# Optimization experiments

Hardware: AMD Instinct MI355X
Metric: run time of the kernel (lower is better)

## Reference

```python
import jax, jax.numpy as jnp
import numpy as np

DILATED_KS = (7, 7)   # dilated_kernel_size (Hk, Wk)
SCALING = 1.0
GROUPS = 1
STRIDE = (1, 1)
PADDING = (3, 3)


def construct_kernel(weight, P):
    """Bilinear scatter-add of kernel_count weighted points into a dense
    (out, in//g, Hk, Wk) kernel. weight: (O, Cg, K), P: (2, Cg, K)."""
    Hk, Wk = DILATED_KS
    lim_h, lim_w = Hk // 2, Wk // 2
    O, Cg, K = weight.shape
    ph = jnp.clip(P[0] * SCALING, -lim_h, lim_h) + lim_h    # (Cg, K) in [0, Hk-1]
    pw = jnp.clip(P[1] * SCALING, -lim_w, lim_w) + lim_w    # (Cg, K) in [0, Wk-1]
    ih = jnp.floor(ph).astype(jnp.int32)
    iw = jnp.floor(pw).astype(jnp.int32)
    rh = ph - ih
    rw = pw - iw
    cidx = jnp.broadcast_to(jnp.arange(Cg)[:, None], (Cg, K))
    kern = jnp.zeros((O, Cg, Hk, Wk), dtype=weight.dtype)
    corners = [(0, 0, (1 - rh) * (1 - rw)),
               (0, 1, (1 - rh) * rw),
               (1, 0, rh * (1 - rw)),
               (1, 1, rh * rw)]
    for di, dj, frac in corners:
        # out-of-range corners (at the boundary) have zero frac; 'drop' discards them
        kern = kern.at[:, cidx, ih + di, iw + dj].add(weight * frac[None], mode='drop')
    return kern


def setup_inputs() -> dict:
    key = jax.random.key(0)
    k1, k2, k3, k4 = jax.random.split(key, 4)
    x = jax.random.normal(k1, (32, 128, 56, 56), dtype=jnp.float32)
    weight = jax.random.normal(k2, (128, 128, 9), dtype=jnp.float32) * 0.05
    P = jax.random.normal(k3, (2, 128, 9), dtype=jnp.float32)  # positions ~ N(0,1), clamped in fwd
    bias = jax.random.normal(k4, (128,), dtype=jnp.float32) * 0.05
    return {"x": x, "weight": weight, "P": P, "bias": bias}


def reference(x, weight, P, bias):
    kern = construct_kernel(weight, P)  # (O, Cg, 7, 7)
    out = jax.lax.conv_general_dilated(
        x, kern,
        window_strides=STRIDE,
        padding=[(PADDING[0], PADDING[0]), (PADDING[1], PADDING[1])],
        dimension_numbers=('NCHW', 'OIHW', 'NCHW'),
        feature_group_count=GROUPS)
    return out + bias[None, :, None, None]
```

## Files before the change

### kernel.cpp

```cpp
#include <hip/hip_runtime.h>
#include <stdint.h>

typedef short v8s __attribute__((ext_vector_type(8)));
typedef float v4f __attribute__((ext_vector_type(4)));

#define KS    7
#define KPTS  9
#define OCH   128
#define CCH   128
#define NB    32
#define HW    56
#define PAD   3

#define HBLK  4
#define ROWS  10
#define WP    72
#define CCK   32
#define NCC   4
#define HP    62
#define ROWB  (WP*CCK*2)
#define XS_B  (ROWS*WP*CCK*2)
#define AB_B  (4*OCH*CCK*2)
#define SMEM_B (XS_B + AB_B)
#define KB_BYTES ((size_t)NCC*49*OCH*CCK*2)

__device__ __forceinline__ unsigned short f2bf(float f) {
  unsigned int u = __builtin_bit_cast(unsigned int, f);
  u += 0x7fffu + ((u >> 16) & 1u);
  return (unsigned short)(u >> 16);
}

__device__ __forceinline__ void gl_lds16(const void* g, void* l) {
  __builtin_amdgcn_global_load_lds(
      (const __attribute__((address_space(1))) unsigned int*)g,
      (__attribute__((address_space(3))) unsigned int*)l, 16, 0, 0);
}

__global__ __launch_bounds__(128) void build_kern(
    const float* __restrict__ wgt, const float* __restrict__ P,
    unsigned short* __restrict__ kb) {
  __shared__ float sm[OCH*49];
  const int c = blockIdx.x, o = threadIdx.x;
  float* mine = &sm[o*49];
  #pragma unroll
  for (int j = 0; j < 49; ++j) mine[j] = 0.f;
  for (int k = 0; k < KPTS; ++k) {
    const float ph = fminf(fmaxf(P[c*KPTS + k], -3.f), 3.f) + 3.f;
    const float pw = fminf(fmaxf(P[CCH*KPTS + c*KPTS + k], -3.f), 3.f) + 3.f;
    const int ih = (int)floorf(ph), iw = (int)floorf(pw);
    const float rh = ph - (float)ih, rw = pw - (float)iw;
    const float wt = wgt[(o*CCH + c)*KPTS + k];
    mine[ih*KS + iw] += wt*(1.f-rh)*(1.f-rw);
    if (iw+1 < KS) mine[ih*KS + iw+1] += wt*(1.f-rh)*rw;
    if (ih+1 < KS) mine[(ih+1)*KS + iw] += wt*rh*(1.f-rw);
    if (ih+1 < KS && iw+1 < KS) mine[(ih+1)*KS + iw+1] += wt*rh*rw;
  }
  const int cc = c >> 5, sc = (c >> 3) & 3, cl = c & 7;
  const int pc = sc ^ ((o >> 1) & 3);
  for (int tap = 0; tap < 49; ++tap)
    kb[(((size_t)(cc*49 + tap)*OCH + o)*CCK) + pc*8 + cl] = f2bf(mine[tap]);
}

__global__ __launch_bounds__(256) void xpose(const float* __restrict__ x,
                                             unsigned short* __restrict__ xt) {
  __shared__ unsigned short lb[CCK][HW + 2];
  const int hp = blockIdx.x;
  const int cc = blockIdx.y;
  const int n  = blockIdx.z;
  const int t  = threadIdx.x;
  const int h  = hp - PAD;
  const bool valid = (unsigned)h < (unsigned)HW;
  if (valid) {
    const float* xb = x + ((size_t)(n*CCH + cc*CCK)*HW + h)*HW;
    #pragma unroll
    for (int k = 0; k < 7; ++k) {
      const int j = k*256 + t;
      const int c = j / HW, w = j % HW;
      lb[c][w] = f2bf(xb[(size_t)c*HW*HW + w]);
    }
  }
  __syncthreads();
  unsigned short* orow = xt + (size_t)((n*NCC + cc)*HP + hp)*(WP*CCK);
  for (int q = t; q < WP*4; q += 256) {
    const int wq = q >> 2, pc = q & 3;
    const int s  = pc ^ ((wq >> 1) & 3);
    v8s v = (v8s){0,0,0,0,0,0,0,0};
    const int w = wq - PAD;
    if (valid && (unsigned)w < (unsigned)HW) {
      #pragma unroll
      for (int jj = 0; jj < 8; ++jj) v[jj] = (short)lb[s*8 + jj][w];
    }
    *(v8s*)&orow[wq*CCK + pc*8] = v;
  }
}

#define MFMA_TAP(FA, FB)                                                      \
  __builtin_amdgcn_s_setprio(1);                                              \
  _Pragma("unroll")                                                           \
  for (int nt = 0; nt < 4; ++nt) {                                            \
    _Pragma("unroll")                                                         \
    for (int mt = 0; mt < 8; ++mt)                                            \
      acc[mt][nt] = __builtin_amdgcn_mfma_f32_16x16x32_bf16(FA[mt], FB[nt],   \
                                                            acc[mt][nt], 0, 0, 0); \
  }                                                                           \
  __builtin_amdgcn_s_setprio(0);

__global__ __launch_bounds__(256, 2) void dcls_conv(
    const unsigned short* __restrict__ xt, const unsigned short* __restrict__ kb,
    const float* __restrict__ bias, float* __restrict__ out)
{
  extern __shared__ char smem[];
  unsigned short* xs = (unsigned short*)smem;
  unsigned short* ab = (unsigned short*)(smem + XS_B);

  const int n   = blockIdx.x;
  const int hb  = blockIdx.y;
  const int tid = threadIdx.x;
  const int lane = tid & 63;
  const int wv   = tid >> 6;
  const int col  = lane & 15;
  const int kgrp = lane >> 4;
  const int swA  = (kgrp ^ ((col >> 1) & 3)) << 3;

  v4f acc[8][4];
  #pragma unroll
  for (int m = 0; m < 8; ++m)
    #pragma unroll
    for (int t = 0; t < 4; ++t)
      acc[m][t] = (v4f){0.f,0.f,0.f,0.f};

  v8s fa0[8], fa1[8], fb0[4], fb1[4];

  for (int cc = 0; cc < NCC; ++cc) {
    const char* src = (const char*)xt + (size_t)((n*NCC + cc)*HP + hb*HBLK)*ROWB;
    for (int i = wv; i < 45; i += 4)
      gl_lds16(src + i*1024 + lane*16, (char*)xs + i*1024);
    const char* ks = (const char*)kb + (size_t)cc*49*8192;
    #pragma unroll
    for (int u = 0; u < 2; ++u)
      #pragma unroll
      for (int j = 0; j < 2; ++j)
        gl_lds16(ks + u*8192 + wv*2048 + j*1024 + lane*16,
                 (char*)ab + u*8192 + wv*2048 + j*1024);
    __syncthreads();

    #pragma unroll
    for (int mt = 0; mt < 8; ++mt)
      fa0[mt] = *(const v8s*)&ab[(mt*16 + col)*CCK + swA];
    {
      const int swB = (kgrp ^ ((col >> 1) & 3)) << 3;
      const int base = (wv*WP + col)*CCK + swB;
      #pragma unroll
      for (int nt = 0; nt < 4; ++nt)
        fb0[nt] = *(const v8s*)&xs[base + nt*512];
    }

    for (int phx = 0; phx < 24; ++phx) {
      const int t0 = 2*phx;
      {
        const int tp = t0 + 2;
        #pragma unroll
        for (int j = 0; j < 2; ++j)
          gl_lds16(ks + (size_t)tp*8192 + wv*2048 + j*1024 + lane*16,
                   (char*)ab + (size_t)(tp & 3)*8192 + wv*2048 + j*1024);
        const int tq = t0 + 3;
        if (tq < 49) {
          #pragma unroll
          for (int j = 0; j < 2; ++j)
            gl_lds16(ks + (size_t)tq*8192 + wv*2048 + j*1024 + lane*16,
                     (char*)ab + (size_t)(tq & 3)*8192 + wv*2048 + j*1024);
        }
      }
      {
        const int t = t0 + 1, kh = t/7, kw = t - kh*7, r = wv + kh;
        const unsigned short* ap = ab + (size_t)(t & 3)*(OCH*CCK);
        #pragma unroll
        for (int mt = 0; mt < 8; ++mt)
          fa1[mt] = *(const v8s*)&ap[(mt*16 + col)*CCK + swA];
        const int swB = (kgrp ^ (((col + kw) >> 1) & 3)) << 3;
        const int base = (r*WP + col + kw)*CCK + swB;
        #pragma unroll
        for (int nt = 0; nt < 4; ++nt)
          fb1[nt] = *(const v8s*)&xs[base + nt*512];
      }
      MFMA_TAP(fa0, fb0)
      {
        const int t = t0 + 2, kh = t/7, kw = t - kh*7, r = wv + kh;
        const int swB = (kgrp ^ (((col + kw) >> 1) & 3)) << 3;
        const int base = (r*WP + col + kw)*CCK + swB;
        #pragma unroll
        for (int nt = 0; nt < 4; ++nt)
          fb0[nt] = *(const v8s*)&xs[base + nt*512];
      }
      MFMA_TAP(fa1, fb1)
      __syncthreads();
      {
        const unsigned short* ap = ab + (size_t)((t0 + 2) & 3)*(OCH*CCK);
        #pragma unroll
        for (int mt = 0; mt < 8; ++mt)
          fa0[mt] = *(const v8s*)&ap[(mt*16 + col)*CCK + swA];
      }
    }
    MFMA_TAP(fa0, fb0)
    __syncthreads();
  }

  const int h = hb*HBLK + wv;
  #pragma unroll
  for (int mt = 0; mt < 8; ++mt) {
    #pragma unroll
    for (int rr = 0; rr < 4; ++rr) {
      const int o = mt*16 + (lane >> 4)*4 + rr;
      const float bs = bias[o];
      #pragma unroll
      for (int nt = 0; nt < 4; ++nt) {
        const int w = nt*16 + col;
        if (w < HW)
          out[((size_t)(n*OCH + o)*HW + h)*HW + w] = acc[mt][nt][rr] + bs;
      }
    }
  }
}

extern "C" void kernel_launch(void* const* d_in, const int* in_sizes, int n_in,
                              void* d_out, int out_size, void* d_ws, size_t ws_size,
                              hipStream_t stream) {
  const float* x    = (const float*)d_in[0];
  const float* wgt  = (const float*)d_in[1];
  const float* P    = (const float*)d_in[2];
  const float* bias = (const float*)d_in[3];
  float* out = (float*)d_out;

  unsigned short* kb = (unsigned short*)d_ws;
  unsigned short* xt = (unsigned short*)((char*)d_ws + (2u<<20));

  hipFuncSetAttribute((const void*)dcls_conv,
                      hipFuncAttributeMaxDynamicSharedMemorySize, SMEM_B);

  build_kern<<<CCH, OCH, 0, stream>>>(wgt, P, kb);
  xpose<<<dim3(HP, NCC, NB), 256, 0, stream>>>(x, xt);
  dcls_conv<<<dim3(NB, HW/HBLK), 256, SMEM_B, stream>>>(xt, kb, bias, out);
}
```

Measured before the change: 159.3 us.

## Switch conv to 32x32x16 MFMA with 8-wave blocks and register-streamed weights

Replaces the 16x16x32 bf16 MFMA tiling with 32x32x16 MFMA, doubles the rows per block to 8 with 512 threads, and prefetches the per-tap weight fragments straight from global memory into registers in an MFMA-ready layout instead of staging them through LDS with per-tap barriers. The weight builder emits that fragment-ordered layout. The goal is to cut LDS traffic and synchronisation in the inner tap loop and raise MFMA efficiency. The cost is exposed global-load latency on weight fragments, more registers, and only 224 blocks in the grid.

```diff
diff --git a/kernel.cpp b/kernel.cpp
--- a/kernel.cpp
+++ b/kernel.cpp
@@ -1,8 +1,8 @@
 #include <hip/hip_runtime.h>
 #include <stdint.h>
 
-typedef short v8s __attribute__((ext_vector_type(8)));
-typedef float v4f __attribute__((ext_vector_type(4)));
+typedef short v8s  __attribute__((ext_vector_type(8)));
+typedef float v16f __attribute__((ext_vector_type(16)));
 
 #define KS    7
 #define KPTS  9
@@ -12,17 +12,14 @@
 #define HW    56
 #define PAD   3
 
-#define HBLK  4
-#define ROWS  10
+#define HBLK  8
+#define ROWS  14
 #define WP    72
 #define CCK   32
 #define NCC   4
 #define HP    62
 #define ROWB  (WP*CCK*2)
-#define XS_B  (ROWS*WP*CCK*2)
-#define AB_B  (4*OCH*CCK*2)
-#define SMEM_B (XS_B + AB_B)
-#define KB_BYTES ((size_t)NCC*49*OCH*CCK*2)
+#define SMEM_B 65536
 
 __device__ __forceinline__ unsigned short f2bf(float f) {
   unsigned int u = __builtin_bit_cast(unsigned int, f);
@@ -55,10 +52,12 @@
     if (ih+1 < KS) mine[(ih+1)*KS + iw] += wt*rh*(1.f-rw);
     if (ih+1 < KS && iw+1 < KS) mine[(ih+1)*KS + iw+1] += wt*rh*rw;
   }
-  const int cc = c >> 5, sc = (c >> 3) & 3, cl = c & 7;
-  const int pc = sc ^ ((o >> 1) & 3);
+  const int cc = c >> 5, c32 = c & 31;
+  const int ks = c32 >> 4, g = (c32 >> 3) & 1, j = c & 7;
+  const int mt = o >> 5, l5 = o & 31;
+  const size_t base = ((size_t)cc*49*8 + ks*4 + mt)*512 + (g*32 + l5)*8 + j;
   for (int tap = 0; tap < 49; ++tap)
-    kb[(((size_t)(cc*49 + tap)*OCH + o)*CCK) + pc*8 + cl] = f2bf(mine[tap]);
+    kb[base + (size_t)tap*4096] = f2bf(mine[tap]);
 }
 
 __global__ __launch_bounds__(256) void xpose(const float* __restrict__ x,
@@ -94,129 +93,102 @@
   }
 }
 
-#define MFMA_TAP(FA, FB)                                                      \
-  __builtin_amdgcn_s_setprio(1);                                              \
-  _Pragma("unroll")                                                           \
-  for (int nt = 0; nt < 4; ++nt) {                                            \
+#define TAP_BODY(T, CUR, NXT, PF)                                             \
+  {                                                                           \
+    const int kh = (T)/7, kw = (T) - kh*7;                                    \
+    if (PF) {                                                                 \
+      const unsigned short* kn = kt + (size_t)((T)+1)*4096;                   \
+      _Pragma("unroll")                                                       \
+      for (int f = 0; f < 8; ++f)                                             \
+        NXT[f] = *(const v8s*)&kn[f*512 + lane*8];                            \
+    }                                                                         \
+    const int r = wv + kh;                                                    \
+    v8s bf[2][2];                                                             \
     _Pragma("unroll")                                                         \
-    for (int mt = 0; mt < 8; ++mt)                                            \
-      acc[mt][nt] = __builtin_amdgcn_mfma_f32_16x16x32_bf16(FA[mt], FB[nt],   \
-                                                            acc[mt][nt], 0, 0, 0); \
-  }                                                                           \
-  __builtin_amdgcn_s_setprio(0);
-
-__global__ __launch_bounds__(256, 2) void dcls_conv(
+    for (int nt = 0; nt < 2; ++nt) {                                          \
+      const int w = nt*32 + l5 + kw;                                          \
+      const int xw = (w >> 1) & 3;                                            \
+      _Pragma("unroll")                                                       \
+      for (int ks = 0; ks < 2; ++ks) {                                        \
+        const int phys = (ks*2 + g) ^ xw;                                     \
+        bf[nt][ks] = *(const v8s*)&xs[(r*WP + w)*CCK + phys*8];               \
+      }                                                                       \
+    }                                                                         \
+    __builtin_amdgcn_s_setprio(1);                                            \
+    _Pragma("unroll")                                                         \
+    for (int ks = 0; ks < 2; ++ks)                                            \
+      _Pragma("unroll")                                                       \
+      for (int mt = 0; mt < 4; ++mt)                                          \
+        _Pragma("unroll")                                                     \
+        for (int nt = 0; nt < 2; ++nt)                                        \
+          acc[mt][nt] = __builtin_amdgcn_mfma_f32_32x32x16_bf16(              \
+              CUR[ks*4 + mt], bf[nt][ks], acc[mt][nt], 0, 0, 0);              \
+    __builtin_amdgcn_s_setprio(0);                                            \
+  }
+
+__global__ __launch_bounds__(512, 2) void dcls_conv(
     const unsigned short* __restrict__ xt, const unsigned short* __restrict__ kb,
     const float* __restrict__ bias, float* __restrict__ out)
 {
   extern __shared__ char smem[];
   unsigned short* xs = (unsigned short*)smem;
-  unsigned short* ab = (unsigned short*)(smem + XS_B);
 
   const int n   = blockIdx.x;
   const int hb  = blockIdx.y;
   const int tid = threadIdx.x;
   const int lane = tid & 63;
   const int wv   = tid >> 6;
-  const int col  = lane & 15;
-  const int kgrp = lane >> 4;
-  const int swA  = (kgrp ^ ((col >> 1) & 3)) << 3;
-
-  v4f acc[8][4];
-  #pragma unroll
-  for (int m = 0; m < 8; ++m)
-    #pragma unroll
-    for (int t = 0; t < 4; ++t)
-      acc[m][t] = (v4f){0.f,0.f,0.f,0.f};
-
-  v8s fa0[8], fa1[8], fb0[4], fb1[4];
+  const int l5   = lane & 31;
+  const int g    = lane >> 5;
+
+  v16f acc[4][2];
+  {
+    v16f z;
+    #pragma unroll
+    for (int i = 0; i < 16; ++i) z[i] = 0.f;
+    #pragma unroll
+    for (int m = 0; m < 4; ++m)
+      #pragma unroll
+      for (int t = 0; t < 2; ++t)
+        acc[m][t] = z;
+  }
+
+  v8s A0[8], A1[8];
 
   for (int cc = 0; cc < NCC; ++cc) {
+    __syncthreads();
     const char* src = (const char*)xt + (size_t)((n*NCC + cc)*HP + hb*HBLK)*ROWB;
-    for (int i = wv; i < 45; i += 4)
-      gl_lds16(src + i*1024 + lane*16, (char*)xs + i*1024);
-    const char* ks = (const char*)kb + (size_t)cc*49*8192;
-    #pragma unroll
-    for (int u = 0; u < 2; ++u)
-      #pragma unroll
-      for (int j = 0; j < 2; ++j)
-        gl_lds16(ks + u*8192 + wv*2048 + j*1024 + lane*16,
-                 (char*)ab + u*8192 + wv*2048 + j*1024);
+    #pragma unroll
+    for (int q = 0; q < 8; ++q)
+      gl_lds16(src + (wv*8 + q)*1024 + lane*16, (char*)xs + (wv*8 + q)*1024);
+    const unsigned short* kt = kb + (size_t)cc*49*4096;
+    #pragma unroll
+    for (int f = 0; f < 8; ++f)
+      A0[f] = *(const v8s*)&kt[f*512 + lane*8];
     __syncthreads();
 
-    #pragma unroll
-    for (int mt = 0; mt < 8; ++mt)
-      fa0[mt] = *(const v8s*)&ab[(mt*16 + col)*CCK + swA];
-    {
-      const int swB = (kgrp ^ ((col >> 1) & 3)) << 3;
-      const int base = (wv*WP + col)*CCK + swB;
-      #pragma unroll
-      for (int nt = 0; nt < 4; ++nt)
-        fb0[nt] = *(const v8s*)&xs[base + nt*512];
-    }
-
-    for (int phx = 0; phx < 24; ++phx) {
-      const int t0 = 2*phx;
-      {
-        const int tp = t0 + 2;
-        #pragma unroll
-        for (int j = 0; j < 2; ++j)
-          gl_lds16(ks + (size_t)tp*8192 + wv*2048 + j*1024 + lane*16,
-                   (char*)ab + (size_t)(tp & 3)*8192 + wv*2048 + j*1024);
-        const int tq = t0 + 3;
-        if (tq < 49) {
-          #pragma unroll
-          for (int j = 0; j < 2; ++j)
-            gl_lds16(ks + (size_t)tq*8192 + wv*2048 + j*1024 + lane*16,
-                     (char*)ab + (size_t)(tq & 3)*8192 + wv*2048 + j*1024);
-        }
-      }
-      {
-        const int t = t0 + 1, kh = t/7, kw = t - kh*7, r = wv + kh;
-        const unsigned short* ap = ab + (size_t)(t & 3)*(OCH*CCK);
-        #pragma unroll
-        for (int mt = 0; mt < 8; ++mt)
-          fa1[mt] = *(const v8s*)&ap[(mt*16 + col)*CCK + swA];
-        const int swB = (kgrp ^ (((col + kw) >> 1) & 3)) << 3;
-        const int base = (r*WP + col + kw)*CCK + swB;
-        #pragma unroll
-        for (int nt = 0; nt < 4; ++nt)
-          fb1[nt] = *(const v8s*)&xs[base + nt*512];
-      }
-      MFMA_TAP(fa0, fb0)
-      {
-        const int t = t0 + 2, kh = t/7, kw = t - kh*7, r = wv + kh;
-        const int swB = (kgrp ^ (((col + kw) >> 1) & 3)) << 3;
-        const int base = (r*WP + col + kw)*CCK + swB;
-        #pragma unroll
-        for (int nt = 0; nt < 4; ++nt)
-          fb0[nt] = *(const v8s*)&xs[base + nt*512];
-      }
-      MFMA_TAP(fa1, fb1)
-      __syncthreads();
-      {
-        const unsigned short* ap = ab + (size_t)((t0 + 2) & 3)*(OCH*CCK);
-        #pragma unroll
-        for (int mt = 0; mt < 8; ++mt)
-          fa0[mt] = *(const v8s*)&ap[(mt*16 + col)*CCK + swA];
-      }
-    }
-    MFMA_TAP(fa0, fb0)
-    __syncthreads();
+    int t = 0;
+    #pragma unroll 1
+    for (int p = 0; p < 24; ++p) {
+      TAP_BODY(t,     A0, A1, true)
+      TAP_BODY(t + 1, A1, A0, true)
+      t += 2;
+    }
+    TAP_BODY(48, A0, A1, false)
   }
 
   const int h = hb*HBLK + wv;
   #pragma unroll
-  for (int mt = 0; mt < 8; ++mt) {
-    #pragma unroll
-    for (int rr = 0; rr < 4; ++rr) {
-      const int o = mt*16 + (lane >> 4)*4 + rr;
-      const float bs = bias[o];
-      #pragma unroll
-      for (int nt = 0; nt < 4; ++nt) {
-        const int w = nt*16 + col;
-        if (w < HW)
-          out[((size_t)(n*OCH + o)*HW + h)*HW + w] = acc[mt][nt][rr] + bs;
+  for (int mt = 0; mt < 4; ++mt) {
+    #pragma unroll
+    for (int rr = 0; rr < 16; ++rr) {
+      const int o = mt*32 + (rr & 3) + 8*(rr >> 2) + 4*g;
+      const int w = l5;
+      float v0 = acc[mt][0][rr] + bias[o];
+      out[((size_t)(n*OCH + o)*HW + h)*HW + w] = v0;
+      if (l5 < 24) {
+        float v1 = acc[mt][1][rr] + bias[o];
+        out[((size_t)(n*OCH + o)*HW + h)*HW + 32 + l5] = v1;
       }
     }
   }
@@ -239,5 +211,5 @@
 
   build_kern<<<CCH, OCH, 0, stream>>>(wgt, P, kb);
   xpose<<<dim3(HP, NCC, NB), 256, 0, stream>>>(x, xt);
-  dcls_conv<<<dim3(NB, HW/HBLK), 256, SMEM_B, stream>>>(xt, kb, bias, out);
-}
+  dcls_conv<<<dim3(NB, KS), 512, SMEM_B, stream>>>(xt, kb, bias, out);
+}
```

Result: slower. 216.5 us (+35.9%).

## Double conv block height to 8 rows with 512 threads and per-tap barrier pipeline

Applied to the files above, without the earlier changes.

The conv block now computes 8 output rows with 8 waves (512 threads) instead of 4 rows with 4 waves, which halves the grid to 32x7 blocks. The goal is to share each staged kernel tap and input halo across twice as many output rows, cutting global-to-LDS weight traffic per output. The tap loop is also simplified: one tap per iteration, one prefetched tap load, explicit vmcnt waits and a barrier each tap, with no register double-buffering of fragments. The risks are that 224 blocks under-fill the CUs, that there is less cross-block latency hiding, and that the new scheme pays more barriers and exposes LDS load latency.

```diff
diff --git a/kernel.cpp b/kernel.cpp
--- a/kernel.cpp
+++ b/kernel.cpp
@@ -12,8 +12,8 @@
 #define HW    56
 #define PAD   3
 
-#define HBLK  4
-#define ROWS  10
+#define HBLK  8
+#define ROWS  14
 #define WP    72
 #define CCK   32
 #define NCC   4
@@ -22,7 +22,6 @@
 #define XS_B  (ROWS*WP*CCK*2)
 #define AB_B  (4*OCH*CCK*2)
 #define SMEM_B (XS_B + AB_B)
-#define KB_BYTES ((size_t)NCC*49*OCH*CCK*2)
 
 __device__ __forceinline__ unsigned short f2bf(float f) {
   unsigned int u = __builtin_bit_cast(unsigned int, f);
@@ -94,18 +93,32 @@
   }
 }
 
-#define MFMA_TAP(FA, FB)                                                      \
-  __builtin_amdgcn_s_setprio(1);                                              \
-  _Pragma("unroll")                                                           \
-  for (int nt = 0; nt < 4; ++nt) {                                            \
+#define TAP_COMPUTE(T)                                                        \
+  {                                                                           \
+    const int kh = (T)/7, kw = (T) - kh*7;                                    \
+    const int r = wv + kh;                                                    \
+    const unsigned short* ap = ab + (size_t)((T) & 3)*(OCH*CCK);              \
+    v8s a[8], b[4];                                                           \
     _Pragma("unroll")                                                         \
     for (int mt = 0; mt < 8; ++mt)                                            \
-      acc[mt][nt] = __builtin_amdgcn_mfma_f32_16x16x32_bf16(FA[mt], FB[nt],   \
-                                                            acc[mt][nt], 0, 0, 0); \
-  }                                                                           \
-  __builtin_amdgcn_s_setprio(0);
-
-__global__ __launch_bounds__(256, 2) void dcls_conv(
+      a[mt] = *(const v8s*)&ap[(mt*16 + col)*CCK + swA];                      \
+    _Pragma("unroll")                                                         \
+    for (int nt = 0; nt < 4; ++nt) {                                          \
+      const int wp = nt*16 + col + kw;                                        \
+      b[nt] = *(const v8s*)&xs[(r*WP + wp)*CCK +                              \
+                               ((kgrp ^ ((wp >> 1) & 3)) << 3)];              \
+    }                                                                         \
+    __builtin_amdgcn_s_setprio(1);                                            \
+    _Pragma("unroll")                                                         \
+    for (int nt = 0; nt < 4; ++nt)                                            \
+      _Pragma("unroll")                                                       \
+      for (int mt = 0; mt < 8; ++mt)                                          \
+        acc[mt][nt] = __builtin_amdgcn_mfma_f32_16x16x32_bf16(                \
+            a[mt], b[nt], acc[mt][nt], 0, 0, 0);                              \
+    __builtin_amdgcn_s_setprio(0);                                            \
+  }
+
+__global__ __launch_bounds__(512, 2) void dcls_conv(
     const unsigned short* __restrict__ xt, const unsigned short* __restrict__ kb,
     const float* __restrict__ bias, float* __restrict__ out)
 {
@@ -129,80 +142,31 @@
     for (int t = 0; t < 4; ++t)
       acc[m][t] = (v4f){0.f,0.f,0.f,0.f};
 
-  v8s fa0[8], fa1[8], fb0[4], fb1[4];
-
   for (int cc = 0; cc < NCC; ++cc) {
+    __syncthreads();
     const char* src = (const char*)xt + (size_t)((n*NCC + cc)*HP + hb*HBLK)*ROWB;
-    for (int i = wv; i < 45; i += 4)
+    for (int i = wv; i < 63; i += 8)
       gl_lds16(src + i*1024 + lane*16, (char*)xs + i*1024);
     const char* ks = (const char*)kb + (size_t)cc*49*8192;
-    #pragma unroll
-    for (int u = 0; u < 2; ++u)
-      #pragma unroll
-      for (int j = 0; j < 2; ++j)
-        gl_lds16(ks + u*8192 + wv*2048 + j*1024 + lane*16,
-                 (char*)ab + u*8192 + wv*2048 + j*1024);
-    __syncthreads();
-
-    #pragma unroll
-    for (int mt = 0; mt < 8; ++mt)
-      fa0[mt] = *(const v8s*)&ab[(mt*16 + col)*CCK + swA];
-    {
-      const int swB = (kgrp ^ ((col >> 1) & 3)) << 3;
-      const int base = (wv*WP + col)*CCK + swB;
-      #pragma unroll
-      for (int nt = 0; nt < 4; ++nt)
-        fb0[nt] = *(const v8s*)&xs[base + nt*512];
-    }
-
-    for (int phx = 0; phx < 24; ++phx) {
-      const int t0 = 2*phx;
-      {
-        const int tp = t0 + 2;
-        #pragma unroll
-        for (int j = 0; j < 2; ++j)
-          gl_lds16(ks + (size_t)tp*8192 + wv*2048 + j*1024 + lane*16,
-                   (char*)ab + (size_t)(tp & 3)*8192 + wv*2048 + j*1024);
-        const int tq = t0 + 3;
-        if (tq < 49) {
-          #pragma unroll
-          for (int j = 0; j < 2; ++j)
-            gl_lds16(ks + (size_t)tq*8192 + wv*2048 + j*1024 + lane*16,
-                     (char*)ab + (size_t)(tq & 3)*8192 + wv*2048 + j*1024);
-        }
-      }
-      {
-        const int t = t0 + 1, kh = t/7, kw = t - kh*7, r = wv + kh;
-        const unsigned short* ap = ab + (size_t)(t & 3)*(OCH*CCK);
-        #pragma unroll
-        for (int mt = 0; mt < 8; ++mt)
-          fa1[mt] = *(const v8s*)&ap[(mt*16 + col)*CCK + swA];
-        const int swB = (kgrp ^ (((col + kw) >> 1) & 3)) << 3;
-        const int base = (r*WP + col + kw)*CCK + swB;
-        #pragma unroll
-        for (int nt = 0; nt < 4; ++nt)
-          fb1[nt] = *(const v8s*)&xs[base + nt*512];
-      }
-      MFMA_TAP(fa0, fb0)
-      {
-        const int t = t0 + 2, kh = t/7, kw = t - kh*7, r = wv + kh;
-        const int swB = (kgrp ^ (((col + kw) >> 1) & 3)) << 3;
-        const int base = (r*WP + col + kw)*CCK + swB;
-        #pragma unroll
-        for (int nt = 0; nt < 4; ++nt)
-          fb0[nt] = *(const v8s*)&xs[base + nt*512];
-      }
-      MFMA_TAP(fa1, fb1)
-      __syncthreads();
-      {
-        const unsigned short* ap = ab + (size_t)((t0 + 2) & 3)*(OCH*CCK);
-        #pragma unroll
-        for (int mt = 0; mt < 8; ++mt)
-          fa0[mt] = *(const v8s*)&ap[(mt*16 + col)*CCK + swA];
-      }
-    }
-    MFMA_TAP(fa0, fb0)
-    __syncthreads();
+    gl_lds16(ks + wv*1024 + lane*16, (char*)ab + wv*1024 + lane*16);
+    gl_lds16(ks + 8192 + wv*1024 + lane*16, (char*)ab + 8192 + wv*1024 + lane*16);
+    asm volatile("s_waitcnt vmcnt(0)" ::: "memory");
+    __builtin_amdgcn_s_barrier();
+
+    #pragma unroll 1
+    for (int T = 0; T < 47; ++T) {
+      gl_lds16(ks + (size_t)(T + 2)*8192 + wv*1024 + lane*16,
+               (char*)ab + (size_t)((T + 2) & 3)*8192 + wv*1024 + lane*16);
+      asm volatile("s_waitcnt vmcnt(2)" ::: "memory");
+      __builtin_amdgcn_s_barrier();
+      TAP_COMPUTE(T)
+    }
+    asm volatile("s_waitcnt vmcnt(1)" ::: "memory");
+    __builtin_amdgcn_s_barrier();
+    TAP_COMPUTE(47)
+    asm volatile("s_waitcnt vmcnt(0)" ::: "memory");
+    __builtin_amdgcn_s_barrier();
+    TAP_COMPUTE(48)
   }
 
   const int h = hb*HBLK + wv;
@@ -239,5 +203,5 @@
 
   build_kern<<<CCH, OCH, 0, stream>>>(wgt, P, kb);
   xpose<<<dim3(HP, NCC, NB), 256, 0, stream>>>(x, xt);
-  dcls_conv<<<dim3(NB, HW/HBLK), 256, SMEM_B, stream>>>(xt, kb, bias, out);
-}
+  dcls_conv<<<dim3(NB, KS), 512, SMEM_B, stream>>>(xt, kb, bias, out);
+}
```

New measurement: 179.5 us. 1.13x slower.
